# Performance work log

Hardware: AMD Instinct MI355X
Metric: run time of the kernel (lower is better)

Reference implementation:

```python
import jax, jax.numpy as jnp
import numpy as np

D_MODEL = 256
N_HEADS = 8
N_LEVELS = 4
N_POINTS = 4
SHAPES = np.array([[64, 64], [32, 32], [16, 16], [8, 8]], dtype=np.int32)


def setup_inputs() -> dict:
    key = jax.random.key(0)
    ks = jax.random.split(key, 10)
    Lq = int((SHAPES[:, 0] * SHAPES[:, 1]).sum())  # 5440
    N, d = 8, D_MODEL
    noff = N_HEADS * N_LEVELS * N_POINTS * 2
    nw = N_HEADS * N_LEVELS * N_POINTS
    s = 1.0 / np.sqrt(d).astype(np.float32)
    inp = {
        'query': jax.random.normal(ks[0], (N, Lq, d), jnp.float32),
        'reference_points': jax.random.uniform(ks[1], (N, Lq, N_LEVELS, 2), jnp.float32),
        'spatial_shapes': jnp.asarray(SHAPES),
        'level_start_index': jnp.asarray(np.concatenate([[0], np.cumsum(SHAPES[:, 0] * SHAPES[:, 1])[:-1]]).astype(np.int32)),
        'W_value': jax.random.normal(ks[2], (d, d), jnp.float32) * s,
        'b_value': jnp.zeros((d,), jnp.float32),
        'W_off': jax.random.normal(ks[3], (d, noff), jnp.float32) * 0.01,
        'b_off': jax.random.uniform(ks[4], (noff,), jnp.float32, minval=-0.5, maxval=0.5),
        'W_attn': jax.random.normal(ks[5], (d, nw), jnp.float32) * s,
        'b_attn': jnp.zeros((nw,), jnp.float32),
        'W_out': jax.random.normal(ks[6], (d, d), jnp.float32) * s,
        'b_out': jnp.zeros((d,), jnp.float32),
    }
    return inp


def _bilinear_sample(val_l, loc_l, H, W):
    # val_l: [N, h, H*W, dh] flattened level feature map
    # loc_l: [N, Lq, h, P, 2] normalized (x, y) in [0, 1]
    # grid_sample semantics, align_corners=False, zero padding
    N, h, HW, dh = val_l.shape
    Lq, P = loc_l.shape[1], loc_l.shape[3]
    x = loc_l[..., 0] * W - 0.5
    y = loc_l[..., 1] * H - 0.5
    x0 = jnp.floor(x)
    y0 = jnp.floor(y)
    wx = (x - x0)[..., None]  # [N, Lq, h, P, 1]
    wy = (y - y0)[..., None]
    x0i = x0.astype(jnp.int32)
    y0i = y0.astype(jnp.int32)

    def gather(yi, xi):
        valid = (xi >= 0) & (xi < W) & (yi >= 0) & (yi < H)  # [N, Lq, h, P]
        idx = jnp.clip(yi, 0, H - 1) * W + jnp.clip(xi, 0, W - 1)
        idx = idx.transpose(0, 2, 1, 3).reshape(N, h, Lq * P)  # [N, h, Lq*P]
        g = jnp.take_along_axis(val_l, jnp.broadcast_to(idx[..., None], (N, h, Lq * P, dh)), axis=2)
        g = g.reshape(N, h, Lq, P, dh)
        mask = valid.transpose(0, 2, 1, 3)[..., None].astype(val_l.dtype)
        return g * mask

    v00 = gather(y0i, x0i)
    v01 = gather(y0i, x0i + 1)
    v10 = gather(y0i + 1, x0i)
    v11 = gather(y0i + 1, x0i + 1)
    wxt = wx.transpose(0, 2, 1, 3, 4)  # [N, h, Lq, P, 1]
    wyt = wy.transpose(0, 2, 1, 3, 4)
    return (v00 * (1 - wxt) * (1 - wyt) + v01 * wxt * (1 - wyt)
            + v10 * (1 - wxt) * wyt + v11 * wxt * wyt)  # [N, h, Lq, P, dh]


def reference(query, reference_points, spatial_shapes, level_start_index,
              W_value, b_value, W_off, b_off, W_attn, b_attn, W_out, b_out):
    shapes = np.asarray(spatial_shapes)  # static level shapes
    N, Lq, d = query.shape
    h, L, P = N_HEADS, N_LEVELS, N_POINTS
    dh = d // h

    v = query @ W_value + b_value  # value_proj (source reassigns query = value_proj(query))
    off = (v @ W_off + b_off).reshape(N, Lq, h, L, P, 2)
    aw = jax.nn.softmax((v @ W_attn + b_attn).reshape(N, Lq, h, L * P), axis=-1)
    aw = aw.reshape(N, Lq, h, L, P)

    # offset_normalizer = [W_l, H_l]
    norm = jnp.asarray(np.stack([shapes[:, 1], shapes[:, 0]], -1), dtype=v.dtype)  # [L, 2]
    loc = reference_points[:, :, None, :, None, :] + off / norm[None, None, None, :, None, :]

    val = v.reshape(N, Lq, h, dh).transpose(0, 2, 1, 3)  # [N, h, Lv, dh]
    out = jnp.zeros((N, h, Lq, dh), v.dtype)
    start = 0
    for l in range(L):
        H, W = int(shapes[l, 0]), int(shapes[l, 1])
        val_l = val[:, :, start:start + H * W]
        sampled = _bilinear_sample(val_l, loc[:, :, :, l], H, W)  # [N, h, Lq, P, dh]
        w_l = aw[:, :, :, l].transpose(0, 2, 1, 3)[..., None]  # [N, h, Lq, P, 1]
        out = out + (sampled * w_l).sum(axis=3)
        start += H * W

    out = out.transpose(0, 2, 1, 3).reshape(N, Lq, d)
    return out @ W_out + b_out
```

## Files before the change

kernel.cpp:

```cpp
#include <hip/hip_runtime.h>
#include <hip/hip_bf16.h>
#include <cstdint>
#include <cstddef>

#define NB 8
#define LQ 5440
#define MROWS (NB * LQ)

typedef __attribute__((ext_vector_type(8))) _Float16       f16x8;
typedef __attribute__((ext_vector_type(4))) float          f32x4;
typedef __attribute__((ext_vector_type(8))) unsigned short ushort8_t;

__device__ __forceinline__ unsigned short f2h(float f) {
    _Float16 h = (_Float16)f;
    unsigned short u;
    __builtin_memcpy(&u, &h, 2);
    return u;
}
__device__ __forceinline__ float h2f(unsigned short u) {
    _Float16 h;
    __builtin_memcpy(&h, &u, 2);
    return (float)h;
}

__device__ __forceinline__ void async16(const void* g, void* l) {
    __builtin_amdgcn_global_load_lds(
        (const __attribute__((address_space(1))) void*)g,
        (__attribute__((address_space(3))) void*)l,
        16, 0, 0);
}

__device__ __forceinline__ void xcd_tile(int& bx, int& by) {
    const int nx   = gridDim.x;
    const int nwg  = nx * gridDim.y;
    const int orig = blockIdx.y * nx + blockIdx.x;
    const int q = nwg >> 3, r = nwg & 7;
    const int xcd = orig & 7, pos = orig >> 3;
    const int nw = (xcd < r ? xcd * (q + 1) : r * (q + 1) + (xcd - r) * q) + pos;
    bx = nw % nx;
    by = nw / nx;
}

__global__ __launch_bounds__(256) void prep_weights(
    const float* __restrict__ Wv, const float* __restrict__ Woff,
    const float* __restrict__ Wat, const float* __restrict__ Wo,
    unsigned short* __restrict__ bigBt,
    unsigned short* __restrict__ Wv16n,
    unsigned short* __restrict__ WoaT,
    unsigned short* __restrict__ WoT)
{
    const int id = blockIdx.x * 256 + threadIdx.x;
    if (id < 65536) {
        const int n = id >> 8, k = id & 255;
        bigBt[id] = f2h(Wv[k * 256 + n]);
    } else if (id < 131072) {
        const int p = id - 65536;
        Wv16n[p] = f2h(Wv[p]);
    } else if (id < 131072 + 98304) {
        const int p = id - 131072;
        const int n = p >> 8, k = p & 255;
        WoaT[p] = (n < 256) ? f2h(Woff[k * 256 + n])
                            : f2h(Wat[k * 128 + (n - 256)]);
    } else {
        const int p = id - (131072 + 98304);
        const int n = p >> 8, k = p & 255;
        WoT[p] = f2h(Wo[k * 256 + n]);
    }
}

__global__ __launch_bounds__(256) void convert_q16(
    const float* __restrict__ q, unsigned short* __restrict__ q16)
{
    const int idx = blockIdx.x * 256 + threadIdx.x;
    const float4 a = reinterpret_cast<const float4*>(q)[idx * 2];
    const float4 b = reinterpret_cast<const float4*>(q)[idx * 2 + 1];
    ushort8_t u;
    u[0] = f2h(a.x); u[1] = f2h(a.y); u[2] = f2h(a.z); u[3] = f2h(a.w);
    u[4] = f2h(b.x); u[5] = f2h(b.y); u[6] = f2h(b.z); u[7] = f2h(b.w);
    reinterpret_cast<ushort8_t*>(q16)[idx] = u;
}

__global__ __launch_bounds__(256) void combine_bias(
    const float* __restrict__ b_value, const float* __restrict__ Woff,
    const float* __restrict__ Wat, const float* __restrict__ b_off,
    const float* __restrict__ b_attn,
    float* __restrict__ fbias, float* __restrict__ zb)
{
    const int b = blockIdx.x;
    const int t = threadIdx.x;
    if (b < 256) {
        if (t == 0) fbias[b] = b_value[b];
        return;
    }
    if (b >= 640) {
        const int i = (b - 640) * 256 + t;
        if (i < 384) zb[i] = 0.f;
        return;
    }
    const int n = b - 256;
    float p = b_value[t] * ((n < 256) ? Woff[t * 256 + n]
                                      : Wat[t * 128 + (n - 256)]);
    for (int o = 32; o >= 1; o >>= 1) p += __shfl_xor(p, o);
    __shared__ float red[4];
    if ((t & 63) == 0) red[t >> 6] = p;
    __syncthreads();
    if (t == 0) {
        float s = red[0] + red[1] + red[2] + red[3];
        fbias[b] = s + ((n < 256) ? b_off[n] : b_attn[n - 256]);
    }
}

#define GEMM_PRE()                                                            \
    __shared__ unsigned short As[128 * 32];                                   \
    __shared__ unsigned short Bs[128 * 32];                                   \
    int bxi, byi;                                                             \
    xcd_tile(bxi, byi);                                                       \
    const int bm = byi * 128;                                                 \
    const int bn = bxi * 128;                                                 \
    const int t    = threadIdx.x;                                             \
    const int lane = t & 63;                                                  \
    const int wid  = t >> 6;                                                  \
    const int wm   = (wid >> 1) * 64;                                         \
    const int wn   = (wid & 1) * 64;                                          \
    const int c    = lane & 15;                                               \
    const int qq   = lane >> 4;                                               \
    const int rA0  = (wid << 5) + (lane >> 2);                                \
    const int rA1  = rA0 + 16;                                                \
    const int kqA0 = (lane & 3) ^ ((rA0 >> 1) & 3);                           \
    const int kqA1 = (lane & 3) ^ ((rA1 >> 1) & 3);                           \
    const unsigned goffA0 = ((unsigned)(bm + rA0) * 256 + kqA0 * 8) * 2;      \
    const unsigned goffA1 = ((unsigned)(bm + rA1) * 256 + kqA1 * 8) * 2;      \
    const unsigned goffB0 = ((unsigned)(bn + rA0) * 256 + kqA0 * 8) * 2;      \
    const unsigned goffB1 = ((unsigned)(bn + rA1) * 256 + kqA1 * 8) * 2;      \
    unsigned short* lA0 = As + (wid << 10);                                   \
    unsigned short* lA1 = lA0 + 512;                                          \
    unsigned short* lB0 = Bs + (wid << 10);                                   \
    unsigned short* lB1 = lB0 + 512;                                          \
    int aoff[4], boff[4];                                                     \
    _Pragma("unroll")                                                         \
    for (int i = 0; i < 4; ++i) {                                             \
        const int ra = wm + i * 16 + c;                                       \
        aoff[i] = ra * 64 + ((qq ^ ((ra >> 1) & 3)) << 4);                    \
        const int rb = wn + i * 16 + c;                                       \
        boff[i] = rb * 64 + ((qq ^ ((rb >> 1) & 3)) << 4);                    \
    }                                                                         \
    f32x4 acc[4][4];                                                          \
    _Pragma("unroll")                                                         \
    for (int i = 0; i < 4; ++i)                                               \
        _Pragma("unroll")                                                     \
        for (int j = 0; j < 4; ++j)                                           \
            acc[i][j] = (f32x4){0.f, 0.f, 0.f, 0.f};

#define GEMM_KLOOP(Atp, Btp)                                                  \
    _Pragma("unroll")                                                         \
    for (int ks = 0; ks < 8; ++ks) {                                          \
        const unsigned kb = ks * 64;                                          \
        async16((const char*)(Atp) + goffA0 + kb, lA0);                       \
        async16((const char*)(Atp) + goffA1 + kb, lA1);                       \
        async16((const char*)(Btp) + goffB0 + kb, lB0);                       \
        async16((const char*)(Btp) + goffB1 + kb, lB1);                       \
        __syncthreads();                                                      \
        f16x8 af[4], bf[4];                                                   \
        _Pragma("unroll")                                                     \
        for (int i = 0; i < 4; ++i)                                           \
            af[i] = *reinterpret_cast<const f16x8*>(                          \
                reinterpret_cast<const char*>(As) + aoff[i]);                 \
        _Pragma("unroll")                                                     \
        for (int j = 0; j < 4; ++j)                                           \
            bf[j] = *reinterpret_cast<const f16x8*>(                          \
                reinterpret_cast<const char*>(Bs) + boff[j]);                 \
        _Pragma("unroll")                                                     \
        for (int i = 0; i < 4; ++i)                                           \
            _Pragma("unroll")                                                 \
            for (int j = 0; j < 4; ++j)                                       \
                acc[i][j] = __builtin_amdgcn_mfma_f32_16x16x32_f16(           \
                    af[i], bf[j], acc[i][j], 0, 0, 0);                        \
        if (ks < 7) __syncthreads();                                          \
    }

template<bool F16_OUT>
__global__ __launch_bounds__(256) void gemm_mfma(
    const unsigned short* __restrict__ At, const unsigned short* __restrict__ Bt,
    const float* __restrict__ bias0, const float* __restrict__ bias1,
    void* __restrict__ C0, void* __restrict__ C1,
    int cs0, int cs1, int split)
{
    GEMM_PRE();
    GEMM_KLOOP(At, Bt);

#pragma unroll
    for (int j = 0; j < 4; ++j) {
        const int col    = bn + wn + j * 16 + c;
        const bool second = col >= split;
        const int ccol   = second ? col - split : col;
        const float bv   = second ? bias1[ccol] : bias0[ccol];
#pragma unroll
        for (int i = 0; i < 4; ++i) {
#pragma unroll
            for (int r = 0; r < 4; ++r) {
                const int row = bm + wm + i * 16 + qq * 4 + r;
                const float v0 = acc[i][j][r] + bv;
                if (F16_OUT) {
                    const float v1 = __shfl_xor(v0, 1);
                    if ((lane & 1) == 0) {
                        const unsigned int packed =
                            (unsigned int)f2h(v0) | ((unsigned int)f2h(v1) << 16);
                        unsigned short* Cb = (unsigned short*)(second ? C1 : C0);
                        const int cs = second ? cs1 : cs0;
                        *reinterpret_cast<unsigned int*>(
                            Cb + (size_t)row * cs + ccol) = packed;
                    }
                } else {
                    float* Cf = (float*)C0;
                    Cf[(size_t)row * cs0 + col] = v0;
                }
            }
        }
    }
}

__global__ __launch_bounds__(256) void gemm_front(
    const unsigned short* __restrict__ At, const unsigned short* __restrict__ Bt,
    const float* __restrict__ fbias,
    unsigned short* __restrict__ v16, unsigned short* __restrict__ off16,
    unsigned short* __restrict__ at16)
{
    GEMM_PRE();
    GEMM_KLOOP(At, Bt);

#pragma unroll
    for (int j = 0; j < 4; ++j) {
        const int col  = bn + wn + j * 16 + c;
        const float bv = fbias[col];
#pragma unroll
        for (int i = 0; i < 4; ++i) {
#pragma unroll
            for (int r = 0; r < 4; ++r) {
                const int row = bm + wm + i * 16 + qq * 4 + r;
                const float v0 = acc[i][j][r] + bv;
                const float v1 = __shfl_xor(v0, 1);
                if ((lane & 1) == 0) {
                    const unsigned int packed =
                        (unsigned int)f2h(v0) | ((unsigned int)f2h(v1) << 16);
                    unsigned short* dst;
                    if (col < 256)      dst = v16   + (size_t)row * 256 + col;
                    else if (col < 512) dst = off16 + (size_t)row * 256 + (col - 256);
                    else                dst = at16  + (size_t)row * 128 + (col - 512);
                    *reinterpret_cast<unsigned int*>(dst) = packed;
                }
            }
        }
    }
}

__global__ __launch_bounds__(256) void sample_kernel(
    const unsigned short* __restrict__ v16,
    const unsigned short* __restrict__ off16,
    const unsigned short* __restrict__ attn16,
    const float* __restrict__ refpts,
    unsigned short* __restrict__ pre16)
{
    const int lane = threadIdx.x & 63;
    const int wv   = threadIdx.x >> 6;
    const int bid  = (blockIdx.x & 7) * 1360 + (blockIdx.x >> 3);
    const int row  = bid * 4 + wv;
    const int n    = row / LQ;

    __shared__ uint4 swi[4][328];

    const ushort4 o4 = reinterpret_cast<const ushort4*>(off16)[(size_t)row * 64 + lane];
    const unsigned int lg = reinterpret_cast<const unsigned int*>(attn16)[(size_t)row * 64 + lane];
    const float l0 = h2f((unsigned short)(lg & 0xffff));
    const float l1 = h2f((unsigned short)(lg >> 16));

    const int h   = lane >> 3;
    const int k   = lane & 7;
    const int lev = k >> 1;
    const float rx = refpts[(size_t)row * 8 + lev * 2 + 0];
    const float ry = refpts[(size_t)row * 8 + lev * 2 + 1];

    float m = fmaxf(l0, l1);
    m = fmaxf(m, __shfl_xor(m, 1));
    m = fmaxf(m, __shfl_xor(m, 2));
    m = fmaxf(m, __shfl_xor(m, 4));
    const float e0 = __expf(l0 - m);
    const float e1 = __expf(l1 - m);
    float s = e0 + e1;
    s += __shfl_xor(s, 1);
    s += __shfl_xor(s, 2);
    s += __shfl_xor(s, 4);
    const float inv = 1.f / s;

    const int  W     = 64 >> lev;
    const int  start = (lev == 0) ? 0 : (lev == 1) ? 4096 : (lev == 2) ? 5120 : 5376;
    const float rs   = 0.015625f * (float)(1 << lev);

#pragma unroll
    for (int pp = 0; pp < 2; ++pp) {
        const float lx = rx + h2f(pp ? o4.z : o4.x) * rs;
        const float ly = ry + h2f(pp ? o4.w : o4.y) * rs;
        const float wgt = (pp ? e1 : e0) * inv;

        const float x = lx * (float)W - 0.5f;
        const float y = ly * (float)W - 0.5f;
        const float fx = floorf(x), fy = floorf(y);
        const int xi = (int)fx, yi = (int)fy;
        const float wx = x - fx, wy = y - fy;

        const int x0 = min(max(xi, 0), W - 1);
        const int x1 = min(max(xi + 1, 0), W - 1);
        const int y0 = min(max(yi, 0), W - 1);
        const int y1 = min(max(yi + 1, 0), W - 1);
        const float vx0 = (xi >= 0 && xi < W)         ? (1.f - wx) : 0.f;
        const float vx1 = (xi + 1 >= 0 && xi + 1 < W) ? wx         : 0.f;
        const float vy0 = (yi >= 0 && yi < W)         ? (1.f - wy) : 0.f;
        const float vy1 = (yi + 1 >= 0 && yi + 1 < W) ? wy         : 0.f;

        const int hb  = h * 64;
        const unsigned int b00 = (unsigned int)((start + y0 * W + x0) * 512 + hb);
        const unsigned int b01 = (unsigned int)((start + y0 * W + x1) * 512 + hb);
        const unsigned int b10 = (unsigned int)((start + y1 * W + x0) * 512 + hb);
        const unsigned int b11 = (unsigned int)((start + y1 * W + x1) * 512 + hb);

        uint4 c0, c1;
        c0.x = __float_as_uint(wgt * vy0 * vx0);
        c0.y = __float_as_uint(wgt * vy0 * vx1);
        c0.z = b00; c0.w = b01;
        c1.x = __float_as_uint(wgt * vy1 * vx0);
        c1.y = __float_as_uint(wgt * vy1 * vx1);
        c1.z = b10; c1.w = b11;
        const int base = h * 41 + 5 * k + 2 * pp;
        swi[wv][base + 0] = c0;
        swi[wv][base + 1] = c1;
    }
    __syncthreads();

    const int cp = (lane >> 2) & 1;
    const int cg = lane & 3;
    const unsigned int koff = cg * 16;

    const int nu = __builtin_amdgcn_readfirstlane(n);
    const char* vn = reinterpret_cast<const char*>(v16) + (size_t)nu * (LQ * 512);
    const uint4* wib = &swi[wv][h * 41 + cp];

#define OFS(j) (2 * (j) + ((j) >> 1))
#define GLD(o) (*reinterpret_cast<const ushort8_t*>(vn + ((o) + koff)))

    float acc[8];
#pragma unroll
    for (int i = 0; i < 8; ++i) acc[i] = 0.f;

    uint4 wi0 = wib[OFS(0)];
    uint4 wi1 = wib[OFS(1)];
    uint4 wi2 = wib[OFS(2)];
    uint4 wi3 = wi2;
    ushort8_t va0 = GLD(wi0.z), vb0 = GLD(wi0.w);
    ushort8_t va1 = GLD(wi1.z), vb1 = GLD(wi1.w);
    ushort8_t va2 = va1,        vb2 = vb1;

#pragma unroll
    for (int j = 0; j < 16; ++j) {
        if (j <= 13) { va2 = GLD(wi2.z); vb2 = GLD(wi2.w); }
        if (j <= 12) wi3 = wib[OFS(j + 3)];

        const float wa = __uint_as_float(wi0.x);
        const float wb = __uint_as_float(wi0.y);
#pragma unroll
        for (int i = 0; i < 8; ++i)
            acc[i] = fmaf(h2f(va0[i]), wa, acc[i]);
#pragma unroll
        for (int i = 0; i < 8; ++i)
            acc[i] = fmaf(h2f(vb0[i]), wb, acc[i]);

        wi0 = wi1; wi1 = wi2; wi2 = wi3;
        va0 = va1; va1 = va2; vb0 = vb1; vb1 = vb2;
    }
#undef OFS
#undef GLD

#pragma unroll
    for (int i = 0; i < 8; ++i)
        acc[i] += __shfl_xor(acc[i], 4);

    if (cp == 0) {
        ushort8_t st;
#pragma unroll
        for (int i = 0; i < 8; ++i) st[i] = f2h(acc[i]);
        *reinterpret_cast<ushort8_t*>(
            pre16 + (size_t)row * 256 + h * 32 + cg * 8) = st;
    }
}

extern "C" void kernel_launch(void* const* d_in, const int* in_sizes, int n_in,
                              void* d_out, int out_size, void* d_ws, size_t ws_size,
                              hipStream_t stream)
{
    const float* query   = (const float*)d_in[0];
    const float* refpts  = (const float*)d_in[1];
    const float* W_value = (const float*)d_in[4];
    const float* b_value = (const float*)d_in[5];
    const float* W_off   = (const float*)d_in[6];
    const float* b_off   = (const float*)d_in[7];
    const float* W_attn  = (const float*)d_in[8];
    const float* b_attn  = (const float*)d_in[9];
    const float* W_out   = (const float*)d_in[10];
    const float* b_out   = (const float*)d_in[11];
    float* out = (float*)d_out;

    unsigned short* ws_v16   = (unsigned short*)d_ws;
    unsigned short* ws_off16 = ws_v16   + (size_t)MROWS * 256;
    unsigned short* ws_at16  = ws_off16 + (size_t)MROWS * 256;
    unsigned short* ws_pre16 = ws_at16  + (size_t)MROWS * 128;
    unsigned short* ws_q16   = ws_pre16 + (size_t)MROWS * 256;
    unsigned short* ws_bigBt = ws_q16   + (size_t)MROWS * 256;
    unsigned short* ws_wv16n = ws_bigBt + 640 * 256;
    unsigned short* ws_woaT  = ws_wv16n + 65536;
    unsigned short* ws_woT   = ws_woaT  + 98304;
    float*          ws_fbias = (float*)(ws_woT + 65536);
    float*          ws_zb    = ws_fbias + 640;

    prep_weights<<<dim3(1152), 256, 0, stream>>>(
        W_value, W_off, W_attn, W_out, ws_bigBt, ws_wv16n, ws_woaT, ws_woT);

    combine_bias<<<dim3(642), 256, 0, stream>>>(
        b_value, W_off, W_attn, b_off, b_attn, ws_fbias, ws_zb);

    convert_q16<<<dim3(5440), 256, 0, stream>>>(query, ws_q16);

    gemm_mfma<true><<<dim3(2, 3), 256, 0, stream>>>(
        ws_woaT, ws_wv16n, ws_zb, ws_zb,
        ws_bigBt + 65536, ws_bigBt + 65536, 256, 256, 1 << 30);

    gemm_front<<<dim3(5, 340), 256, 0, stream>>>(
        ws_q16, ws_bigBt, ws_fbias, ws_v16, ws_off16, ws_at16);

    sample_kernel<<<dim3(MROWS / 4), 256, 0, stream>>>(
        ws_v16, ws_off16, ws_at16, refpts, ws_pre16);

    gemm_mfma<false><<<dim3(2, 340), 256, 0, stream>>>(
        ws_pre16, ws_woT, b_out, b_out, out, out, 256, 256, 1 << 30);
}
```

Before: 147.7 us.

## Replace LDS-staged GEMM with direct global-to-register MFMA loads on smaller tiles

The GEMM kernels no longer stage A and B tiles through shared memory with async global-to-LDS copies and barriers. Each wave now loads its MFMA fragments straight from global memory, and the block tile shrinks from 128x128 to 128x64, which doubles the grid. This removes LDS traffic and the per-step __syncthreads, and gives more blocks to fill the GPU. In exchange there is no cross-wave reuse of B through LDS, so redundant global or L2 loads increase, and the fragment loads are strided rather than coalesced.

```diff
diff --git a/kernel.cpp b/kernel.cpp
--- a/kernel.cpp
+++ b/kernel.cpp
@@ -21,13 +21,6 @@
     _Float16 h;
     __builtin_memcpy(&h, &u, 2);
     return (float)h;
-}
-
-__device__ __forceinline__ void async16(const void* g, void* l) {
-    __builtin_amdgcn_global_load_lds(
-        (const __attribute__((address_space(1))) void*)g,
-        (__attribute__((address_space(3))) void*)l,
-        16, 0, 0);
 }
 
 __device__ __forceinline__ void xcd_tile(int& bx, int& by) {
@@ -110,96 +103,68 @@
     }
 }
 
-#define GEMM_PRE()                                                            \
-    __shared__ unsigned short As[128 * 32];                                   \
-    __shared__ unsigned short Bs[128 * 32];                                   \
+#define GEMM_CORE()                                                           \
     int bxi, byi;                                                             \
     xcd_tile(bxi, byi);                                                       \
     const int bm = byi * 128;                                                 \
-    const int bn = bxi * 128;                                                 \
-    const int t    = threadIdx.x;                                             \
-    const int lane = t & 63;                                                  \
-    const int wid  = t >> 6;                                                  \
-    const int wm   = (wid >> 1) * 64;                                         \
-    const int wn   = (wid & 1) * 64;                                          \
+    const int bn = bxi * 64;                                                  \
+    const int lane = threadIdx.x & 63;                                        \
+    const int wid  = threadIdx.x >> 6;                                        \
     const int c    = lane & 15;                                               \
     const int qq   = lane >> 4;                                               \
-    const int rA0  = (wid << 5) + (lane >> 2);                                \
-    const int rA1  = rA0 + 16;                                                \
-    const int kqA0 = (lane & 3) ^ ((rA0 >> 1) & 3);                           \
-    const int kqA1 = (lane & 3) ^ ((rA1 >> 1) & 3);                           \
-    const unsigned goffA0 = ((unsigned)(bm + rA0) * 256 + kqA0 * 8) * 2;      \
-    const unsigned goffA1 = ((unsigned)(bm + rA1) * 256 + kqA1 * 8) * 2;      \
-    const unsigned goffB0 = ((unsigned)(bn + rA0) * 256 + kqA0 * 8) * 2;      \
-    const unsigned goffB1 = ((unsigned)(bn + rA1) * 256 + kqA1 * 8) * 2;      \
-    unsigned short* lA0 = As + (wid << 10);                                   \
-    unsigned short* lA1 = lA0 + 512;                                          \
-    unsigned short* lB0 = Bs + (wid << 10);                                   \
-    unsigned short* lB1 = lB0 + 512;                                          \
-    int aoff[4], boff[4];                                                     \
+    const int wr   = bm + wid * 32;                                           \
+    const unsigned short* pa0 = At + (size_t)(wr + c) * 256 + qq * 8;         \
+    const unsigned short* pa1 = pa0 + 16 * 256;                               \
+    const unsigned short* pb0 = Bt + (size_t)(bn + c) * 256 + qq * 8;         \
+    const unsigned short* pb1 = pb0 + 16 * 256;                               \
+    const unsigned short* pb2 = pb0 + 32 * 256;                               \
+    const unsigned short* pb3 = pb0 + 48 * 256;                               \
+    f32x4 acc[2][4];                                                          \
     _Pragma("unroll")                                                         \
-    for (int i = 0; i < 4; ++i) {                                             \
-        const int ra = wm + i * 16 + c;                                       \
-        aoff[i] = ra * 64 + ((qq ^ ((ra >> 1) & 3)) << 4);                    \
-        const int rb = wn + i * 16 + c;                                       \
-        boff[i] = rb * 64 + ((qq ^ ((rb >> 1) & 3)) << 4);                    \
-    }                                                                         \
-    f32x4 acc[4][4];                                                          \
-    _Pragma("unroll")                                                         \
-    for (int i = 0; i < 4; ++i)                                               \
+    for (int s = 0; s < 2; ++s)                                               \
         _Pragma("unroll")                                                     \
         for (int j = 0; j < 4; ++j)                                           \
-            acc[i][j] = (f32x4){0.f, 0.f, 0.f, 0.f};
-
-#define GEMM_KLOOP(Atp, Btp)                                                  \
+            acc[s][j] = (f32x4){0.f, 0.f, 0.f, 0.f};                          \
     _Pragma("unroll")                                                         \
     for (int ks = 0; ks < 8; ++ks) {                                          \
-        const unsigned kb = ks * 64;                                          \
-        async16((const char*)(Atp) + goffA0 + kb, lA0);                       \
-        async16((const char*)(Atp) + goffA1 + kb, lA1);                       \
-        async16((const char*)(Btp) + goffB0 + kb, lB0);                       \
-        async16((const char*)(Btp) + goffB1 + kb, lB1);                       \
-        __syncthreads();                                                      \
-        f16x8 af[4], bf[4];                                                   \
-        _Pragma("unroll")                                                     \
-        for (int i = 0; i < 4; ++i)                                           \
-            af[i] = *reinterpret_cast<const f16x8*>(                          \
-                reinterpret_cast<const char*>(As) + aoff[i]);                 \
-        _Pragma("unroll")                                                     \
-        for (int j = 0; j < 4; ++j)                                           \
-            bf[j] = *reinterpret_cast<const f16x8*>(                          \
-                reinterpret_cast<const char*>(Bs) + boff[j]);                 \
-        _Pragma("unroll")                                                     \
-        for (int i = 0; i < 4; ++i)                                           \
-            _Pragma("unroll")                                                 \
-            for (int j = 0; j < 4; ++j)                                       \
-                acc[i][j] = __builtin_amdgcn_mfma_f32_16x16x32_f16(           \
-                    af[i], bf[j], acc[i][j], 0, 0, 0);                        \
-        if (ks < 7) __syncthreads();                                          \
+        const int o = ks * 32;                                                \
+        const f16x8 a0 = *reinterpret_cast<const f16x8*>(pa0 + o);            \
+        const f16x8 a1 = *reinterpret_cast<const f16x8*>(pa1 + o);            \
+        const f16x8 b0 = *reinterpret_cast<const f16x8*>(pb0 + o);            \
+        const f16x8 b1 = *reinterpret_cast<const f16x8*>(pb1 + o);            \
+        const f16x8 b2 = *reinterpret_cast<const f16x8*>(pb2 + o);            \
+        const f16x8 b3 = *reinterpret_cast<const f16x8*>(pb3 + o);            \
+        acc[0][0] = __builtin_amdgcn_mfma_f32_16x16x32_f16(a0, b0, acc[0][0], 0, 0, 0); \
+        acc[0][1] = __builtin_amdgcn_mfma_f32_16x16x32_f16(a0, b1, acc[0][1], 0, 0, 0); \
+        acc[0][2] = __builtin_amdgcn_mfma_f32_16x16x32_f16(a0, b2, acc[0][2], 0, 0, 0); \
+        acc[0][3] = __builtin_amdgcn_mfma_f32_16x16x32_f16(a0, b3, acc[0][3], 0, 0, 0); \
+        acc[1][0] = __builtin_amdgcn_mfma_f32_16x16x32_f16(a1, b0, acc[1][0], 0, 0, 0); \
+        acc[1][1] = __builtin_amdgcn_mfma_f32_16x16x32_f16(a1, b1, acc[1][1], 0, 0, 0); \
+        acc[1][2] = __builtin_amdgcn_mfma_f32_16x16x32_f16(a1, b2, acc[1][2], 0, 0, 0); \
+        acc[1][3] = __builtin_amdgcn_mfma_f32_16x16x32_f16(a1, b3, acc[1][3], 0, 0, 0); \
     }
 
 template<bool F16_OUT>
-__global__ __launch_bounds__(256) void gemm_mfma(
+__global__ __launch_bounds__(256) void gemm_direct(
     const unsigned short* __restrict__ At, const unsigned short* __restrict__ Bt,
     const float* __restrict__ bias0, const float* __restrict__ bias1,
     void* __restrict__ C0, void* __restrict__ C1,
     int cs0, int cs1, int split)
 {
-    GEMM_PRE();
-    GEMM_KLOOP(At, Bt);
+    GEMM_CORE();
 
 #pragma unroll
     for (int j = 0; j < 4; ++j) {
-        const int col    = bn + wn + j * 16 + c;
+        const int col    = bn + j * 16 + c;
         const bool second = col >= split;
         const int ccol   = second ? col - split : col;
         const float bv   = second ? bias1[ccol] : bias0[ccol];
 #pragma unroll
-        for (int i = 0; i < 4; ++i) {
+        for (int s = 0; s < 2; ++s) {
 #pragma unroll
             for (int r = 0; r < 4; ++r) {
-                const int row = bm + wm + i * 16 + qq * 4 + r;
-                const float v0 = acc[i][j][r] + bv;
+                const int row = wr + s * 16 + qq * 4 + r;
+                const float v0 = acc[s][j][r] + bv;
                 if (F16_OUT) {
                     const float v1 = __shfl_xor(v0, 1);
                     if ((lane & 1) == 0) {
@@ -225,19 +190,18 @@
     unsigned short* __restrict__ v16, unsigned short* __restrict__ off16,
     unsigned short* __restrict__ at16)
 {
-    GEMM_PRE();
-    GEMM_KLOOP(At, Bt);
+    GEMM_CORE();
 
 #pragma unroll
     for (int j = 0; j < 4; ++j) {
-        const int col  = bn + wn + j * 16 + c;
+        const int col  = bn + j * 16 + c;
         const float bv = fbias[col];
 #pragma unroll
-        for (int i = 0; i < 4; ++i) {
+        for (int s = 0; s < 2; ++s) {
 #pragma unroll
             for (int r = 0; r < 4; ++r) {
-                const int row = bm + wm + i * 16 + qq * 4 + r;
-                const float v0 = acc[i][j][r] + bv;
+                const int row = wr + s * 16 + qq * 4 + r;
+                const float v0 = acc[s][j][r] + bv;
                 const float v1 = __shfl_xor(v0, 1);
                 if ((lane & 1) == 0) {
                     const unsigned int packed =
@@ -427,16 +391,16 @@
 
     convert_q16<<<dim3(5440), 256, 0, stream>>>(query, ws_q16);
 
-    gemm_mfma<true><<<dim3(2, 3), 256, 0, stream>>>(
+    gemm_direct<true><<<dim3(4, 3), 256, 0, stream>>>(
         ws_woaT, ws_wv16n, ws_zb, ws_zb,
         ws_bigBt + 65536, ws_bigBt + 65536, 256, 256, 1 << 30);
 
-    gemm_front<<<dim3(5, 340), 256, 0, stream>>>(
+    gemm_front<<<dim3(10, 340), 256, 0, stream>>>(
         ws_q16, ws_bigBt, ws_fbias, ws_v16, ws_off16, ws_at16);
 
     sample_kernel<<<dim3(MROWS / 4), 256, 0, stream>>>(
         ws_v16, ws_off16, ws_at16, refpts, ws_pre16);
 
-    gemm_mfma<false><<<dim3(2, 340), 256, 0, stream>>>(
+    gemm_direct<false><<<dim3(4, 340), 256, 0, stream>>>(
         ws_pre16, ws_woT, b_out, b_out, out, out, 256, 256, 1 << 30);
 }
```

Result: slower. 202.5 us (+37.1%).
